# Performance work log

Measured on AMD Instinct MI355X. Metric: run time of the kernel, lower is better.

The kernel has to match this reference:

```python
import jax, jax.numpy as jnp
import numpy as np

B, T, D, H = 2, 2048, 1024, 16
HD = D // H
EPS = 1e-5


def setup_inputs() -> dict:
    key = jax.random.key(0)
    ks = jax.random.split(key, 6)
    scale = 0.02
    return {
        "x": jax.random.normal(ks[0], (B, T, D), dtype=jnp.float32),
        "wq": jax.random.normal(ks[1], (D, D), dtype=jnp.float32) * scale,
        "bq": jnp.zeros((D,), dtype=jnp.float32),
        "wk": jax.random.normal(ks[2], (D, D), dtype=jnp.float32) * scale,
        "bk": jnp.zeros((D,), dtype=jnp.float32),
        "wv": jax.random.normal(ks[3], (D, D), dtype=jnp.float32) * scale,
        "bv": jnp.zeros((D,), dtype=jnp.float32),
        "wg": jax.random.normal(ks[4], (D, D), dtype=jnp.float32) * scale,
        "bg": jnp.zeros((D,), dtype=jnp.float32),
        "gamma": jnp.ones((D,), dtype=jnp.float32),
        "beta": jnp.zeros((D,), dtype=jnp.float32),
    }


def reference(x, wq, bq, wk, bk, wv, bv, wg, bg, gamma, beta):
    b, t, d = x.shape
    # projections (torch Linear: y = x @ W^T + b, W stored as (out, in))
    def proj(w, bias):
        return jnp.einsum('btd,ed->bte', x, w) + bias
    q = proj(wq, bq).reshape(b, t, H, HD).swapaxes(1, 2)  # b h t hd
    k = proj(wk, bk).reshape(b, t, H, HD).swapaxes(1, 2)
    v = proj(wv, bv).reshape(b, t, H, HD).swapaxes(1, 2)
    # full (non-causal) attention as in the source
    scores = jnp.einsum('bhqd,bhkd->bhqk', q, k) / jnp.sqrt(jnp.float32(HD))
    attn = jax.nn.softmax(scores, axis=-1)
    out = jnp.einsum('bhqk,bhkd->bhqd', attn, v)
    out = out.swapaxes(1, 2).reshape(b, t, d)  # b t (h hd)
    gate = proj(wg, bg)
    y = gate * out
    # GroupNorm with n_heads groups over the channel (d_model) dim, per token
    yg = y.reshape(b, t, H, HD)
    mu = jnp.mean(yg, axis=-1, keepdims=True)
    var = jnp.var(yg, axis=-1, keepdims=True)
    yn = (yg - mu) / jnp.sqrt(var + EPS)
    yn = yn * gamma.reshape(H, HD) + beta.reshape(H, HD)
    return yn.reshape(b, t, d)
```

## Files before the change

### kernel.cpp

```cpp
#include <hip/hip_runtime.h>
#include <hip/hip_bf16.h>
#include <math.h>

namespace {
constexpr int kB = 2, kT = 2048, kD = 1024, kH = 16, kHD = 64;
}

typedef __attribute__((ext_vector_type(8))) short short8;
typedef __attribute__((ext_vector_type(4))) float f32x4;
typedef __attribute__((ext_vector_type(16))) float f32x16;

#if __has_builtin(__builtin_amdgcn_exp2f)
#define EXP2F(x) __builtin_amdgcn_exp2f(x)
#else
#define EXP2F(x) __expf((x) * 0.6931471805599453f)
#endif

__device__ __forceinline__ ushort f2bf(float f) {
  union { float f; uint u; } c; c.f = f;
  uint u = c.u + 0x7FFFu + ((c.u >> 16) & 1u);
  return (ushort)(u >> 16);
}

__device__ __forceinline__ float bf2f(ushort u) {
  union { uint u; float f; } c; c.u = ((uint)u) << 16; return c.f;
}

__device__ __forceinline__ uint pack_bf2(float a, float b) {
  uint r;
  asm("v_cvt_pk_bf16_f32 %0, %1, %2" : "=v"(r) : "v"(a), "v"(b));
  return r;
}

__device__ __forceinline__ void gload_lds16(const void* g, void* l) {
  __builtin_amdgcn_global_load_lds(
      (const __attribute__((address_space(1))) void*)g,
      (__attribute__((address_space(3))) void*)l, 16, 0, 0);
}


__global__ __launch_bounds__(256) void cvt_kernel(
    const float* __restrict__ x, const float* __restrict__ w0,
    const float* __restrict__ w1, const float* __restrict__ w2,
    const float* __restrict__ w3, ushort* __restrict__ out)
{
  const size_t g = (size_t)blockIdx.x * 256 + threadIdx.x;
  const size_t e = g * 8;
  const float* src; size_t rel;
  if (e < ((size_t)1 << 22)) { src = x; rel = e; }
  else {
    size_t e2 = e - ((size_t)1 << 22);
    int wi = (int)(e2 >> 20);
    src = wi == 0 ? w0 : wi == 1 ? w1 : wi == 2 ? w2 : w3;
    rel = e2 & (((size_t)1 << 20) - 1);
  }
  float4 v0 = *reinterpret_cast<const float4*>(src + rel);
  float4 v1 = *reinterpret_cast<const float4*>(src + rel + 4);
  union { ushort u[8]; short8 s8; } o;
  o.u[0] = f2bf(v0.x); o.u[1] = f2bf(v0.y); o.u[2] = f2bf(v0.z); o.u[3] = f2bf(v0.w);
  o.u[4] = f2bf(v1.x); o.u[5] = f2bf(v1.y); o.u[6] = f2bf(v1.z); o.u[7] = f2bf(v1.w);
  *reinterpret_cast<short8*>(out + e) = o.s8;
}

__device__ __forceinline__ void stage_half(
    const ushort* __restrict__ src, int row0, int kcol0,
    ushort* ldsbase, int wid, int lane)
{
#pragma unroll
  for (int part = 0; part < 2; ++part) {
    const int c = part * 512 + wid * 64 + lane;
    const int x = c * 16;
    const int o = x ^ (((x >> 7) & 3) << 4);
    const int r = o >> 6;
    const int cb = (o & 63) >> 1;
    gload_lds16(src + (size_t)(row0 + r) * kD + kcol0 + cb, ldsbase + (x >> 1));
  }
}

__device__ __forceinline__ short8 read_frag(const ushort* half, int r, int lg) {
  const int slot = lg ^ ((r >> 1) & 3);
  return *reinterpret_cast<const short8*>(&half[r * 32 + slot * 8]);
}

#define PH_BAR() do { asm volatile("" ::: "memory"); \
  __builtin_amdgcn_s_barrier(); asm volatile("" ::: "memory"); } while (0)

__global__ __launch_bounds__(512, 2) void proj_mfma_kernel(
    const ushort* __restrict__ Xb, const ushort* __restrict__ Wb,
    const float* __restrict__ bq, const float* __restrict__ bk,
    const float* __restrict__ bv, const float* __restrict__ bg,
    ushort* __restrict__ qo, ushort* __restrict__ ko,
    ushort* __restrict__ vt, ushort* __restrict__ go)
{
  const int mat = blockIdx.z;
  const ushort* Wm = Wb + (size_t)mat * 1024 * 1024;
  const float* bias = mat == 0 ? bq : mat == 1 ? bk : mat == 2 ? bv : bg;
  const int m0 = blockIdx.x * 256;
  const int n0g = blockIdx.y * 256;
  const int tid = threadIdx.x;
  const int wid = tid >> 6, lane = tid & 63;
  const int wr = wid >> 2, wc = wid & 3;
  const int wrow = wr * 128, wcol = wc * 64;
  const int lr = lane & 15, lg = lane >> 4;

  __shared__ ushort lds[65536];

  f32x4 acc[8][4];
#pragma unroll
  for (int i = 0; i < 8; ++i)
#pragma unroll
    for (int j = 0; j < 4; ++j) acc[i][j] = (f32x4){0.f, 0.f, 0.f, 0.f};

  short8 bfr[4];

#define STAGE_A(bu, h, kt) stage_half(Xb, m0,  (kt) * 64 + (h) * 32, \
    &lds[(bu) * 32768 + (h) * 8192], wid, lane)
#define STAGE_B(bu, h, kt) stage_half(Wm, n0g, (kt) * 64 + (h) * 32, \
    &lds[(bu) * 32768 + 16384 + (h) * 8192], wid, lane)

#define PHASE(bu, h, MB, READB, STAGE_STMT, DOVM)                          \
  {                                                                        \
    const ushort* Ah = &lds[(bu) * 32768 + (h) * 8192];                    \
    const ushort* Bh = &lds[(bu) * 32768 + 16384 + (h) * 8192];            \
    short8 af[4];                                                          \
    af[0] = read_frag(Ah, wrow + (MB + 0) * 16 + lr, lg);                  \
    af[1] = read_frag(Ah, wrow + (MB + 1) * 16 + lr, lg);                  \
    af[2] = read_frag(Ah, wrow + (MB + 2) * 16 + lr, lg);                  \
    af[3] = read_frag(Ah, wrow + (MB + 3) * 16 + lr, lg);                  \
    if (READB) {                                                           \
      bfr[0] = read_frag(Bh, wcol + 0 * 16 + lr, lg);                      \
      bfr[1] = read_frag(Bh, wcol + 1 * 16 + lr, lg);                      \
      bfr[2] = read_frag(Bh, wcol + 2 * 16 + lr, lg);                      \
      bfr[3] = read_frag(Bh, wcol + 3 * 16 + lr, lg);                      \
    }                                                                      \
    STAGE_STMT;                                                            \
    PH_BAR();                                                              \
    __builtin_amdgcn_s_setprio(1);                                         \
    _Pragma("unroll")                                                      \
    for (int m2 = 0; m2 < 4; ++m2)                                         \
      _Pragma("unroll")                                                    \
      for (int ni = 0; ni < 4; ++ni)                                       \
        acc[(MB) + m2][ni] = __builtin_amdgcn_mfma_f32_16x16x32_bf16(      \
            af[m2], bfr[ni], acc[(MB) + m2][ni], 0, 0, 0);                 \
    __builtin_amdgcn_s_setprio(0);                                         \
    if (DOVM) asm volatile("s_waitcnt vmcnt(4)" ::: "memory");             \
    PH_BAR();                                                              \
  }

  STAGE_A(0, 0, 0); STAGE_B(0, 0, 0);
  STAGE_A(0, 1, 0); STAGE_B(0, 1, 0);
  STAGE_A(1, 0, 1); STAGE_B(1, 0, 1);
  asm volatile("s_waitcnt vmcnt(4)" ::: "memory");
  PH_BAR();

#pragma unroll 1
  for (int it = 0; it < 8; ++it) {
    const int ta = 2 * it, tb = 2 * it + 1;
    const int tn0 = (ta + 2) & 15;
    const int tn1 = (tb + 2) & 15;
    PHASE(0, 0, 0, 1, (STAGE_A(1, 1, tb)),  0)
    PHASE(0, 0, 4, 0, (STAGE_B(1, 1, tb)),  0)
    PHASE(0, 1, 0, 1, (STAGE_A(0, 0, tn0)), 0)
    PHASE(0, 1, 4, 0, (STAGE_B(0, 0, tn0)), 1)
    PHASE(1, 0, 0, 1, (STAGE_A(0, 1, tn0)), 0)
    PHASE(1, 0, 4, 0, (STAGE_B(0, 1, tn0)), 0)
    PHASE(1, 1, 0, 1, (STAGE_A(1, 0, tn1)), 0)
    PHASE(1, 1, 4, 0, (STAGE_B(1, 0, tn1)), 1)
  }

#undef PHASE
#undef STAGE_A
#undef STAGE_B

  const float vsc = (mat == 0) ? 0.18033688f : 1.0f;

#pragma unroll
  for (int mi = 0; mi < 8; ++mi) {
    const int mbase = m0 + wrow + mi * 16 + 4 * lg;
    const int b = mbase >> 11, t0r = mbase & (kT - 1);
#pragma unroll
    for (int ni = 0; ni < 4; ++ni) {
      const int n = n0g + wcol + ni * 16 + lr;
      const float bn = bias[n];
      if (mat == 3) {
#pragma unroll
        for (int r = 0; r < 4; ++r)
          go[(size_t)(mbase + r) * kD + n] = f2bf(acc[mi][ni][r] + bn);
      } else if (mat == 2) {
        const int h = n >> 6, hd = n & 63;
        const int bh2 = b * kH + h;
        const int nh = hd >> 5, lv = hd & 31;
        const int kc = t0r >> 5, kk0 = t0r & 31;
        const int jf = kk0 >> 4, hi2 = (kk0 >> 3) & 1, jj0 = kk0 & 7;
        const int lane2 = lv + hi2 * 32;
        const size_t off =
            (((((size_t)bh2 * 64 + kc) * 2 + nh) * 2 + jf) * 64 + lane2) * 8 + jj0;
        ushort4 u;
        u.x = f2bf(acc[mi][ni][0] + bn); u.y = f2bf(acc[mi][ni][1] + bn);
        u.z = f2bf(acc[mi][ni][2] + bn); u.w = f2bf(acc[mi][ni][3] + bn);
        *reinterpret_cast<ushort4*>(&vt[off]) = u;
      } else if (mat == 1) {
        const int h = n >> 6, hd = n & 63;
        const int bh2 = b * kH + h;
        const int hk = hd >> 4, hi2 = (hd >> 3) & 1, jj = hd & 7;
#pragma unroll
        for (int r = 0; r < 4; ++r) {
          const int t = t0r + r;
          const int kc = t >> 5, kk = t & 31;
          const size_t off =
              ((((size_t)bh2 * 64 + kc) * 4 + hk) * 64 + kk + hi2 * 32) * 8 + jj;
          ko[off] = f2bf(acc[mi][ni][r] + bn);
        }
      } else {
        const int h = n >> 6, hd = n & 63;
        const int bh2 = b * kH + h;
#pragma unroll
        for (int r = 0; r < 4; ++r)
          qo[((size_t)bh2 * kT + t0r + r) * kHD + hd] =
              f2bf((acc[mi][ni][r] + bn) * vsc);
      }
    }
  }
}

__global__ __launch_bounds__(256, 4) void attn_mfma32_kernel(
    const ushort* __restrict__ Qrm, const ushort* __restrict__ Kf,
    const ushort* __restrict__ Vf, ushort* __restrict__ Op,
    float* __restrict__ lsumP)
{
  const int bid = blockIdx.x;
  const int xcd = bid & 7;
  const int j = bid >> 3;
  const int bh = xcd * 4 + (j >> 5);
  const int rem = j & 31;
  const int qt = rem & 15;
  const int ks = rem >> 4;
  const int tid = threadIdx.x, w = tid >> 6, lane = tid & 63;
  const int lq = lane & 31;
  const int hi = lane >> 5;

  __shared__ ushort kvA[4096];
  __shared__ ushort kvB[4096];

  const int q0 = qt * 128 + w * 32;
  short8 aq[4];
#pragma unroll
  for (int hk = 0; hk < 4; ++hk)
    aq[hk] = *reinterpret_cast<const short8*>(
        &Qrm[((size_t)bh * kT + q0 + lq) * kHD + hk * 16 + hi * 8]);

  f32x16 oacc[2];
#pragma unroll
  for (int nh = 0; nh < 2; ++nh)
#pragma unroll
    for (int r = 0; r < 16; ++r) oacc[nh][r] = 0.f;
  float lsum = 0.f;

  const ushort* kbase = Kf + ((size_t)bh * 64 + ks * 32) * 2048;
  const ushort* vbase = Vf + ((size_t)bh * 64 + ks * 32) * 2048;

#define STAGE_KV(dst, t) do {                                               \
    gload_lds16(kbase + (size_t)(t) * 2048 + tid * 8, &dst[tid * 8]);       \
    gload_lds16(vbase + (size_t)(t) * 2048 + tid * 8, &dst[2048 + tid * 8]);\
  } while (0)

#define COMPUTE_KV(buf) do {                                                \
    short8 kf_[4];                                                          \
    _Pragma("unroll")                                                       \
    for (int hk = 0; hk < 4; ++hk)                                          \
      kf_[hk] = *reinterpret_cast<const short8*>(&buf[(hk * 64 + lane) * 8]);\
    short8 vf[2][2];                                                        \
    _Pragma("unroll")                                                       \
    for (int nh = 0; nh < 2; ++nh)                                          \
      _Pragma("unroll")                                                     \
      for (int jf = 0; jf < 2; ++jf)                                        \
        vf[nh][jf] = *reinterpret_cast<const short8*>(                      \
            &buf[2048 + ((nh * 2 + jf) * 64 + lane) * 8]);                  \
    f32x16 s;                                                               \
    _Pragma("unroll")                                                       \
    for (int r = 0; r < 16; ++r) s[r] = 0.f;                                \
    __builtin_amdgcn_s_setprio(1);                                          \
    _Pragma("unroll")                                                       \
    for (int hk = 0; hk < 4; ++hk)                                          \
      s = __builtin_amdgcn_mfma_f32_32x32x16_bf16(kf_[hk], aq[hk], s, 0, 0, 0);\
    __builtin_amdgcn_s_setprio(0);                                          \
    float p[16];                                                            \
    _Pragma("unroll")                                                       \
    for (int r = 0; r < 16; ++r) p[r] = EXP2F(s[r]);                        \
    float t0 = 0.f, t1 = 0.f;                                               \
    _Pragma("unroll")                                                       \
    for (int r = 0; r < 16; r += 2) { t0 += p[r]; t1 += p[r + 1]; }         \
    lsum += t0 + t1;                                                        \
    uint pk[8];                                                             \
    _Pragma("unroll")                                                       \
    for (int m = 0; m < 8; ++m) pk[m] = pack_bf2(p[2 * m], p[2 * m + 1]);   \
    union { uint u[4]; short8 s8; } fa0, fa1;                               \
    {                                                                       \
      auto s0 = __builtin_amdgcn_permlane32_swap(pk[0], pk[2], false, false);\
      auto s1 = __builtin_amdgcn_permlane32_swap(pk[1], pk[3], false, false);\
      auto s2 = __builtin_amdgcn_permlane32_swap(pk[4], pk[6], false, false);\
      auto s3 = __builtin_amdgcn_permlane32_swap(pk[5], pk[7], false, false);\
      fa0.u[0] = s0[0]; fa0.u[2] = s0[1];                                   \
      fa0.u[1] = s1[0]; fa0.u[3] = s1[1];                                   \
      fa1.u[0] = s2[0]; fa1.u[2] = s2[1];                                   \
      fa1.u[1] = s3[0]; fa1.u[3] = s3[1];                                   \
    }                                                                       \
    __builtin_amdgcn_s_setprio(1);                                          \
    oacc[0] = __builtin_amdgcn_mfma_f32_32x32x16_bf16(vf[0][0], fa0.s8, oacc[0], 0, 0, 0);\
    oacc[0] = __builtin_amdgcn_mfma_f32_32x32x16_bf16(vf[0][1], fa1.s8, oacc[0], 0, 0, 0);\
    oacc[1] = __builtin_amdgcn_mfma_f32_32x32x16_bf16(vf[1][0], fa0.s8, oacc[1], 0, 0, 0);\
    oacc[1] = __builtin_amdgcn_mfma_f32_32x32x16_bf16(vf[1][1], fa1.s8, oacc[1], 0, 0, 0);\
    __builtin_amdgcn_s_setprio(0);                                          \
  } while (0)

  STAGE_KV(kvA, 0);
  __syncthreads();

#pragma unroll 1
  for (int kt = 0; kt < 32; kt += 2) {
    if (kt + 1 < 32) STAGE_KV(kvB, kt + 1);
    COMPUTE_KV(kvA);
    __syncthreads();
    if (kt + 2 < 32) STAGE_KV(kvA, kt + 2);
    COMPUTE_KV(kvB);
    __syncthreads();
  }

#undef STAGE_KV
#undef COMPUTE_KV

  lsum += __shfl_xor(lsum, 32);

  const size_t prow = (((size_t)ks * 32 + bh) * kT + (q0 + lq)) * kHD;
#pragma unroll
  for (int nh = 0; nh < 2; ++nh)
#pragma unroll
    for (int g2 = 0; g2 < 4; ++g2) {
      ushort4 u;
      u.x = f2bf(oacc[nh][4 * g2 + 0]);
      u.y = f2bf(oacc[nh][4 * g2 + 1]);
      u.z = f2bf(oacc[nh][4 * g2 + 2]);
      u.w = f2bf(oacc[nh][4 * g2 + 3]);
      *reinterpret_cast<ushort4*>(&Op[prow + nh * 32 + 8 * g2 + 4 * hi]) = u;
    }
  if (hi == 0)
    lsumP[((size_t)ks * 32 + bh) * kT + q0 + lq] = lsum;
}

__global__ __launch_bounds__(256) void gn_kernel(
    const ushort* __restrict__ gb, const ushort* __restrict__ Op,
    const float* __restrict__ lsumP,
    const float* __restrict__ gamma, const float* __restrict__ beta,
    float* __restrict__ out)
{
  const int tid = threadIdx.x;
  const int grp = blockIdx.x * 16 + (tid >> 4);
  const int l16 = tid & 15;
  const int bt = grp >> 4, h = grp & 15;
  const int b = bt >> 11, t = bt & (kT - 1);
  const int bh = b * kH + h;
  const int c0 = l16 * 4;

  float l = 0.f;
  float ov[4] = {0.f, 0.f, 0.f, 0.f};
#pragma unroll
  for (int ks = 0; ks < 2; ++ks) {
    const size_t base = ((size_t)ks * 32 + bh) * kT + t;
    ushort4 o4 = *reinterpret_cast<const ushort4*>(&Op[base * kHD + c0]);
    ov[0] += bf2f(o4.x); ov[1] += bf2f(o4.y);
    ov[2] += bf2f(o4.z); ov[3] += bf2f(o4.w);
    l += lsumP[base];
  }
  const float inv_l = 1.f / l;
  ushort4 g4 = *reinterpret_cast<const ushort4*>(&gb[(size_t)bt * kD + h * kHD + c0]);
  float y[4];
  y[0] = bf2f(g4.x) * ov[0] * inv_l; y[1] = bf2f(g4.y) * ov[1] * inv_l;
  y[2] = bf2f(g4.z) * ov[2] * inv_l; y[3] = bf2f(g4.w) * ov[3] * inv_l;

  float s = y[0] + y[1] + y[2] + y[3];
  float ss = y[0]*y[0] + y[1]*y[1] + y[2]*y[2] + y[3]*y[3];
#pragma unroll
  for (int off = 8; off; off >>= 1) {
    s  += __shfl_xor(s, off);
    ss += __shfl_xor(ss, off);
  }
  const float mean = s * (1.f / 64.f);
  const float var  = ss * (1.f / 64.f) - mean * mean;
  const float inv  = rsqrtf(var + 1e-5f);

  float4 gm = *reinterpret_cast<const float4*>(&gamma[h * kHD + c0]);
  float4 bt4 = *reinterpret_cast<const float4*>(&beta[h * kHD + c0]);
  float4 o;
  o.x = (y[0] - mean) * inv * gm.x + bt4.x;
  o.y = (y[1] - mean) * inv * gm.y + bt4.y;
  o.z = (y[2] - mean) * inv * gm.z + bt4.z;
  o.w = (y[3] - mean) * inv * gm.w + bt4.w;
  *reinterpret_cast<float4*>(&out[(size_t)bt * kD + h * kHD + c0]) = o;
}

extern "C" void kernel_launch(void* const* d_in, const int* in_sizes, int n_in,
                              void* d_out, int out_size, void* d_ws, size_t ws_size,
                              hipStream_t stream) {
  const float* x     = (const float*)d_in[0];
  const float* wq    = (const float*)d_in[1];
  const float* bq    = (const float*)d_in[2];
  const float* wk    = (const float*)d_in[3];
  const float* bk    = (const float*)d_in[4];
  const float* wv    = (const float*)d_in[5];
  const float* bv    = (const float*)d_in[6];
  const float* wg    = (const float*)d_in[7];
  const float* bg    = (const float*)d_in[8];
  const float* gamma = (const float*)d_in[9];
  const float* beta  = (const float*)d_in[10];

  ushort* cb  = (ushort*)d_ws;
  ushort* qb  = cb + (size_t)8388608;
  ushort* kb  = qb + (size_t)4194304;
  ushort* vtb = kb + (size_t)4194304;
  ushort* gb  = vtb + (size_t)4194304;
  ushort* Op  = gb + (size_t)4194304;
  float*  lsumP = (float*)cb;
  float*  out = (float*)d_out;

  const ushort* xb = cb;
  const ushort* wb = cb + (size_t)4194304;

  cvt_kernel<<<4096, 256, 0, stream>>>(x, wq, wk, wv, wg, cb);
  proj_mfma_kernel<<<dim3(16, 4, 4), 512, 0, stream>>>(
      xb, wb, bq, bk, bv, bg, qb, kb, vtb, gb);
  attn_mfma32_kernel<<<1024, 256, 0, stream>>>(qb, kb, vtb, Op, lsumP);
  gn_kernel<<<4096, 256, 0, stream>>>(gb, Op, lsumP, gamma, beta, out);
}
```

Baseline: 101.8 us.

## Replace 8-phase LDS pipeline with simple double-buffered K32 loop in projection GEMM

Replaces the hand-scheduled 8-phase projection GEMM main loop with a plain double-buffered loop over 32-wide K slices. Each slice stages A and B for the next slice and computes all 8x4 MFMAs on the current one, with one __syncthreads per iteration. LDS use halves and the 2-blocks-per-SM occupancy hint in launch_bounds is dropped. The code is simpler, but there is less fine-grained overlap between global-to-LDS loads and MFMA, and there are now 32 full barriers without the explicit vmcnt waits. The loop relies on __syncthreads to wait for the async LDS loads.

```diff
diff --git a/kernel.cpp b/kernel.cpp
--- a/kernel.cpp
+++ b/kernel.cpp
@@ -82,10 +82,7 @@
   return *reinterpret_cast<const short8*>(&half[r * 32 + slot * 8]);
 }
 
-#define PH_BAR() do { asm volatile("" ::: "memory"); \
-  __builtin_amdgcn_s_barrier(); asm volatile("" ::: "memory"); } while (0)
-
-__global__ __launch_bounds__(512, 2) void proj_mfma_kernel(
+__global__ __launch_bounds__(512) void proj_mfma_kernel(
     const ushort* __restrict__ Xb, const ushort* __restrict__ Wb,
     const float* __restrict__ bq, const float* __restrict__ bk,
     const float* __restrict__ bv, const float* __restrict__ bg,
@@ -103,7 +100,7 @@
   const int wrow = wr * 128, wcol = wc * 64;
   const int lr = lane & 15, lg = lane >> 4;
 
-  __shared__ ushort lds[65536];
+  __shared__ ushort lds[32768];
 
   f32x4 acc[8][4];
 #pragma unroll
@@ -111,66 +108,43 @@
 #pragma unroll
     for (int j = 0; j < 4; ++j) acc[i][j] = (f32x4){0.f, 0.f, 0.f, 0.f};
 
-  short8 bfr[4];
-
-#define STAGE_A(bu, h, kt) stage_half(Xb, m0,  (kt) * 64 + (h) * 32, \
-    &lds[(bu) * 32768 + (h) * 8192], wid, lane)
-#define STAGE_B(bu, h, kt) stage_half(Wm, n0g, (kt) * 64 + (h) * 32, \
-    &lds[(bu) * 32768 + 16384 + (h) * 8192], wid, lane)
-
-#define PHASE(bu, h, MB, READB, STAGE_STMT, DOVM)                          \
-  {                                                                        \
-    const ushort* Ah = &lds[(bu) * 32768 + (h) * 8192];                    \
-    const ushort* Bh = &lds[(bu) * 32768 + 16384 + (h) * 8192];            \
-    short8 af[4];                                                          \
-    af[0] = read_frag(Ah, wrow + (MB + 0) * 16 + lr, lg);                  \
-    af[1] = read_frag(Ah, wrow + (MB + 1) * 16 + lr, lg);                  \
-    af[2] = read_frag(Ah, wrow + (MB + 2) * 16 + lr, lg);                  \
-    af[3] = read_frag(Ah, wrow + (MB + 3) * 16 + lr, lg);                  \
-    if (READB) {                                                           \
-      bfr[0] = read_frag(Bh, wcol + 0 * 16 + lr, lg);                      \
-      bfr[1] = read_frag(Bh, wcol + 1 * 16 + lr, lg);                      \
-      bfr[2] = read_frag(Bh, wcol + 2 * 16 + lr, lg);                      \
-      bfr[3] = read_frag(Bh, wcol + 3 * 16 + lr, lg);                      \
-    }                                                                      \
-    STAGE_STMT;                                                            \
-    PH_BAR();                                                              \
-    __builtin_amdgcn_s_setprio(1);                                         \
-    _Pragma("unroll")                                                      \
-    for (int m2 = 0; m2 < 4; ++m2)                                         \
-      _Pragma("unroll")                                                    \
-      for (int ni = 0; ni < 4; ++ni)                                       \
-        acc[(MB) + m2][ni] = __builtin_amdgcn_mfma_f32_16x16x32_bf16(      \
-            af[m2], bfr[ni], acc[(MB) + m2][ni], 0, 0, 0);                 \
-    __builtin_amdgcn_s_setprio(0);                                         \
-    if (DOVM) asm volatile("s_waitcnt vmcnt(4)" ::: "memory");             \
-    PH_BAR();                                                              \
-  }
-
-  STAGE_A(0, 0, 0); STAGE_B(0, 0, 0);
-  STAGE_A(0, 1, 0); STAGE_B(0, 1, 0);
-  STAGE_A(1, 0, 1); STAGE_B(1, 0, 1);
-  asm volatile("s_waitcnt vmcnt(4)" ::: "memory");
-  PH_BAR();
+#define STAGE32(bu, kh) do {                                                \
+    stage_half(Xb, m0,  (kh) * 32, &lds[(bu) * 16384], wid, lane);          \
+    stage_half(Wm, n0g, (kh) * 32, &lds[(bu) * 16384 + 8192], wid, lane);   \
+  } while (0)
+
+  STAGE32(0, 0);
+  __syncthreads();
 
 #pragma unroll 1
-  for (int it = 0; it < 8; ++it) {
-    const int ta = 2 * it, tb = 2 * it + 1;
-    const int tn0 = (ta + 2) & 15;
-    const int tn1 = (tb + 2) & 15;
-    PHASE(0, 0, 0, 1, (STAGE_A(1, 1, tb)),  0)
-    PHASE(0, 0, 4, 0, (STAGE_B(1, 1, tb)),  0)
-    PHASE(0, 1, 0, 1, (STAGE_A(0, 0, tn0)), 0)
-    PHASE(0, 1, 4, 0, (STAGE_B(0, 0, tn0)), 1)
-    PHASE(1, 0, 0, 1, (STAGE_A(0, 1, tn0)), 0)
-    PHASE(1, 0, 4, 0, (STAGE_B(0, 1, tn0)), 0)
-    PHASE(1, 1, 0, 1, (STAGE_A(1, 0, tn1)), 0)
-    PHASE(1, 1, 4, 0, (STAGE_B(1, 0, tn1)), 1)
-  }
-
-#undef PHASE
-#undef STAGE_A
-#undef STAGE_B
+  for (int kh = 0; kh < 32; ++kh) {
+    const int cur = kh & 1;
+    if (kh + 1 < 32) STAGE32(cur ^ 1, kh + 1);
+    const ushort* Ah = &lds[cur * 16384];
+    const ushort* Bh = &lds[cur * 16384 + 8192];
+    short8 bfr[4];
+#pragma unroll
+    for (int ni = 0; ni < 4; ++ni)
+      bfr[ni] = read_frag(Bh, wcol + ni * 16 + lr, lg);
+    __builtin_amdgcn_s_setprio(1);
+#pragma unroll
+    for (int mb = 0; mb < 2; ++mb) {
+      short8 af[4];
+#pragma unroll
+      for (int m2 = 0; m2 < 4; ++m2)
+        af[m2] = read_frag(Ah, wrow + (mb * 4 + m2) * 16 + lr, lg);
+#pragma unroll
+      for (int m2 = 0; m2 < 4; ++m2)
+#pragma unroll
+        for (int ni = 0; ni < 4; ++ni)
+          acc[mb * 4 + m2][ni] = __builtin_amdgcn_mfma_f32_16x16x32_bf16(
+              af[m2], bfr[ni], acc[mb * 4 + m2][ni], 0, 0, 0);
+    }
+    __builtin_amdgcn_s_setprio(0);
+    __syncthreads();
+  }
+
+#undef STAGE32
 
   const float vsc = (mat == 0) ? 0.18033688f : 1.0f;
 
```

New measurement: 104.4 us. +2.5%, slower.
